# Kernel tuning notes

Measured on AMD Instinct MI355X. Metric: run time of the kernel, lower is better.

## Reference

```python
import jax, jax.numpy as jnp
import numpy as np

B, T, K, H = 32, 128, 16, 4   # batch, agents, in_dim, num_heads
A = 2                          # out_dim (action dim)
H1 = H2 = 256
LOG_STD_MIN, LOG_STD_MAX = -20.0, 2.0


def _linear_params(key, out_dim, in_dim, uniform_w=None):
    k1, k2 = jax.random.split(key)
    if uniform_w is not None:
        w = jax.random.uniform(k1, (out_dim, in_dim), minval=-uniform_w, maxval=uniform_w)
        b = jax.random.uniform(k2, (out_dim,), minval=-uniform_w, maxval=uniform_w)
    else:
        bound = 1.0 / np.sqrt(in_dim)
        w = jax.random.uniform(k1, (out_dim, in_dim), minval=-bound, maxval=bound)
        b = jax.random.uniform(k2, (out_dim,), minval=-bound, maxval=bound)
    return w.astype(jnp.float32), b.astype(jnp.float32)


def setup_inputs() -> dict:
    key = jax.random.key(0)
    ks = jax.random.split(key, 10)
    state = jax.random.normal(ks[0], (B, T, K), dtype=jnp.float32)
    eps = jax.random.normal(ks[1], (B, T, A), dtype=jnp.float32)
    Wq, bq = _linear_params(ks[2], K * H, K)
    Wk, bk = _linear_params(ks[3], K * H, K)
    Wv, bv = _linear_params(ks[4], K * H, K)
    W1, b1 = _linear_params(ks[5], H1, K * H + K)
    W2, b2 = _linear_params(ks[6], H2, H1)
    Wmu, bmu = _linear_params(ks[7], A, H2, uniform_w=0.003)
    Wls, bls = _linear_params(ks[8], A, H2, uniform_w=0.003)
    return {"state": state, "eps": eps, "Wq": Wq, "bq": bq, "Wk": Wk, "bk": bk,
            "Wv": Wv, "bv": bv, "W1": W1, "b1": b1, "W2": W2, "b2": b2,
            "Wmu": Wmu, "bmu": bmu, "Wls": Wls, "bls": bls}


def reference(state, eps, Wq, bq, Wk, bk, Wv, bv, W1, b1, W2, b2, Wmu, bmu, Wls, bls):
    b, t, k = state.shape
    h = H
    # rel[b,i,j] = state[b,j] - state[b,i]
    rel = state[:, None, :, :] - state[:, :, None, :]          # (b,t,t,k)
    q = jax.nn.relu(state @ Wq.T + bq).reshape(b, t, h, k)     # (b,t,h,k)
    q = q.transpose(0, 2, 1, 3)                                # (b,h,t,k)
    Kt = jax.nn.relu(rel @ Wk.T + bk).reshape(b, t, t, h, k)   # (b,i,j,h,k)
    V = jax.nn.relu(rel @ Wv.T + bv).reshape(b, t, t, h, k)
    # scores over pairwise keys vs per-agent query; softmax over j (dim=2 in torch)
    s = jnp.einsum('bijhk,bhik->bhij', Kt, q) / jnp.sqrt(jnp.float32(k))
    w = jax.nn.softmax(s, axis=3)                              # softmax over j
    x = jnp.einsum('bhij,bijhk->bhik', w, V)                   # (b,h,t,k)
    x = x.transpose(0, 2, 1, 3).reshape(b, t, h * k)           # (b,t,h*k)
    x = jnp.concatenate([x, state], axis=-1)                   # (b,t,h*k+k)
    x = jax.nn.relu(x @ W1.T + b1)
    x = jax.nn.relu(x @ W2.T + b2)
    mu = jnp.tanh(x @ Wmu.T + bmu)
    log_std = jnp.tanh(x @ Wls.T + bls)
    log_std = LOG_STD_MIN + 0.5 * (LOG_STD_MAX - LOG_STD_MIN) * (log_std + 1.0)
    std = jnp.exp(log_std)
    z = mu + std * eps                                         # rsample
    action = jnp.tanh(z)
    # Normal log_prob with (z-mu)/std == eps, minus tanh correction
    log_prob = (-0.5 * eps * eps - log_std - 0.5 * jnp.log(2.0 * jnp.pi)) \
               - jnp.log(1.0 - action * action + 1e-7)
    log_prob = jnp.sum(log_prob, axis=-1, keepdims=True)
    return action, log_prob
```

## Files before the change

### kernel.cpp

```cpp
#include <hip/hip_runtime.h>
#include <math.h>

#define NB 32
#define NT 128
#define KD 16

#define QG_OFF   0u
#define PKF_OFF  1048576u
#define PVT_OFF  3145728u
#define W1P_OFF  3670016u
#define W2P_OFF  3719168u

typedef float f32x4 __attribute__((ext_vector_type(4)));
typedef short bf16x8 __attribute__((ext_vector_type(8)));
typedef __fp16 f16x2 __attribute__((ext_vector_type(2)));
union U4B8 { uint4 u; bf16x8 h; };
union U4H8 { uint4 u; f16x2 h[4]; };

#define L_PK 0
#define L_PV 34816
#define L_P  52224
#define L_TOT 60928
#define L_X  0
#define L_H1 3584
#define L_H2 12032

__device__ __forceinline__ unsigned short bf16rne(float f) {
    unsigned u = __float_as_uint(f);
    return (unsigned short)((u + 0x7fffu + ((u >> 16) & 1u)) >> 16);
}
__device__ __forceinline__ void unpack8(uint4 u, float* f) {
    f[0] = __uint_as_float(u.x << 16); f[1] = __uint_as_float(u.x & 0xffff0000u);
    f[2] = __uint_as_float(u.y << 16); f[3] = __uint_as_float(u.y & 0xffff0000u);
    f[4] = __uint_as_float(u.z << 16); f[5] = __uint_as_float(u.z & 0xffff0000u);
    f[6] = __uint_as_float(u.w << 16); f[7] = __uint_as_float(u.w & 0xffff0000u);
}
__device__ __forceinline__ f16x2 pkmax(f16x2 a, f16x2 b) {
    f16x2 d;
    asm("v_pk_max_f16 %0, %1, %2" : "=v"(d) : "v"(a), "v"(b));
    return d;
}
#if __has_builtin(__builtin_amdgcn_fdot2)
#define FDOT2(a, b, c) __builtin_amdgcn_fdot2((a), (b), (c), false)
#else
#define FDOT2(a, b, c) ((c) + (float)(a)[0] * (float)(b)[0] + (float)(a)[1] * (float)(b)[1])
#endif

__global__ __launch_bounds__(256) void prep_kernel(
    const float* __restrict__ state,
    const float* __restrict__ Wq, const float* __restrict__ bq,
    const float* __restrict__ Wk, const float* __restrict__ Wv,
    const float* __restrict__ W1, const float* __restrict__ W2,
    char* __restrict__ wsb)
{
    const int blk = blockIdx.x, tid = threadIdx.x;
    float* Qg  = (float*)(wsb + QG_OFF);
    float* PkF = (float*)(wsb + PKF_OFF);
    unsigned short* PvT = (unsigned short*)(wsb + PVT_OFF);

    if (blk < 128) {
        __shared__ float Wl[3][64][17];
        __shared__ float Sl[32][17];
        const int b = blk >> 2, r0 = (blk & 3) * 32;
        for (int idx = tid; idx < 1024; idx += 256) {
            int o = idx >> 4, m = idx & 15;
            Wl[0][o][m] = Wq[idx];
            Wl[1][o][m] = Wk[idx];
            Wl[2][o][m] = Wv[idx];
        }
        for (int idx = tid; idx < 512; idx += 256)
            Sl[idx >> 4][idx & 15] = state[(size_t)(b * NT + r0) * KD + idx];
        __syncthreads();
        const int o = tid & 63, rr = tid >> 6;
        float wqv[16], wkv[16], wvv[16];
        #pragma unroll
        for (int m = 0; m < 16; ++m) {
            wqv[m] = Wl[0][o][m]; wkv[m] = Wl[1][o][m]; wvv[m] = Wl[2][o][m];
        }
        const float bqo = bq[o];
        for (int r = rr; r < 32; r += 4) {
            float aq = bqo, ak = 0.f, av = 0.f;
            #pragma unroll
            for (int m = 0; m < 16; ++m) {
                float s = Sl[r][m];
                aq = fmaf(s, wqv[m], aq);
                ak = fmaf(s, wkv[m], ak);
                av = fmaf(s, wvv[m], av);
            }
            int row = b * NT + r0 + r;
            Qg[row * 64 + o]  = fmaxf(aq, 0.f) * 0.25f;
            PkF[row * 64 + o] = ak;
            __fp16 hv = (__fp16)av;
            PvT[b * 8192 + o * NT + (r0 + r)] = *(unsigned short*)&hv;
        }
    } else if (blk < 140) {
        int fi = (blk - 128) * 256 + tid;
        int l = fi & 63, rest = fi >> 6;
        int t = rest & 15, ks = rest >> 4;
        int n = t * 16 + (l & 15);
        int kb = ks * 32 + (l >> 4) * 8;
        unsigned short v[8];
        #pragma unroll
        for (int j = 0; j < 8; ++j) {
            int k = kb + j;
            v[j] = (k < 80) ? bf16rne(W1[n * 80 + k]) : (unsigned short)0;
        }
        uint4 u;
        u.x = (unsigned)v[0] | ((unsigned)v[1] << 16);
        u.y = (unsigned)v[2] | ((unsigned)v[3] << 16);
        u.z = (unsigned)v[4] | ((unsigned)v[5] << 16);
        u.w = (unsigned)v[6] | ((unsigned)v[7] << 16);
        ((uint4*)(wsb + W1P_OFF))[fi] = u;
    } else {
        int fi = (blk - 140) * 256 + tid;
        int l = fi & 63, rest = fi >> 6;
        int t = rest & 15, ks = rest >> 4;
        int n = t * 16 + (l & 15);
        int kb = ks * 32 + (l >> 4) * 8;
        unsigned short v[8];
        #pragma unroll
        for (int j = 0; j < 8; ++j) v[j] = bf16rne(W2[n * 256 + kb + j]);
        uint4 u;
        u.x = (unsigned)v[0] | ((unsigned)v[1] << 16);
        u.y = (unsigned)v[2] | ((unsigned)v[3] << 16);
        u.z = (unsigned)v[4] | ((unsigned)v[5] << 16);
        u.w = (unsigned)v[6] | ((unsigned)v[7] << 16);
        ((uint4*)(wsb + W2P_OFF))[fi] = u;
    }
}

__global__ __launch_bounds__(512, 4) void actor_kernel(
    const float* __restrict__ state, const float* __restrict__ eps,
    const float* __restrict__ bkg, const float* __restrict__ bvg,
    const float* __restrict__ b1g, const float* __restrict__ b2g,
    const float* __restrict__ Wmu, const float* __restrict__ bmu,
    const float* __restrict__ Wls, const float* __restrict__ bls,
    const char* __restrict__ wsb, float* __restrict__ out)
{
    __shared__ __align__(16) char sm[L_TOT];
    float* smPk = (float*)(sm + L_PK);

    const int tid = threadIdx.x, w = tid >> 6, lane = tid & 63;
    const int bid = blockIdx.x;
    const int b    = (bid & 7) * 4 + ((bid >> 3) >> 4);
    const int tile = (bid >> 3) & 15;
    const int iloc = tile * 8 + w;
    const int row  = b * NT + iloc;
    const int h = lane >> 4, s = lane & 15, h16 = h << 4;
    const int g = h, lr = s;
    const int t0 = 2 * w;
    const int n0 = w * 32 + lr, n1 = n0 + 16;

    const float* Qg  = (const float*)(wsb + QG_OFF);
    const float* PkF = (const float*)(wsb + PKF_OFF);

    float qA[16], bkr[16];
    {
        const float4* qa  = (const float4*)(Qg + (size_t)row * 64 + h16);
        const float4* bk4 = (const float4*)(bkg + h16);
        #pragma unroll
        for (int q4 = 0; q4 < 4; ++q4) {
            float4 a = qa[q4], k4 = bk4[q4];
            qA[q4*4+0]=a.x; qA[q4*4+1]=a.y; qA[q4*4+2]=a.z; qA[q4*4+3]=a.w;
            bkr[q4*4+0]=k4.x; bkr[q4*4+1]=k4.y; bkr[q4*4+2]=k4.z; bkr[q4*4+3]=k4.w;
        }
    }
    const float bvo = bvg[lane];
    float stt = 0.f;
    if (tid < 128)
        stt = state[((size_t)b * NT + tile * 8 + (tid >> 4)) * KD + (tid & 15)];

    {
        const uint4* srcK = (const uint4*)(PkF + (size_t)b * NT * 64);
        #pragma unroll
        for (int it = 0; it < 4; ++it) {
            int idx = tid + it * 512;
            int r = idx >> 4, c = idx & 15;
            *(uint4*)(smPk + r * 68 + c * 4) = srcK[idx];
        }
        const uint4* srcV = (const uint4*)(wsb + PVT_OFF) + (size_t)b * 1024;
        #pragma unroll
        for (int it = 0; it < 2; ++it) {
            int idx = tid + it * 512;
            int o = idx >> 4, c = idx & 15;
            *(uint4*)(sm + L_PV + o * 272 + c * 16) = srcV[idx];
        }
    }
    __syncthreads();

    float mbeff[16], dotc = 0.f;
    {
        const float* pkI = smPk + iloc * 68 + h16;
        #pragma unroll
        for (int k = 0; k < 16; ++k) {
            float pk = pkI[k];
            mbeff[k] = pk - bkr[k];
            dotc = fmaf(qA[k], bkr[k] - pk, dotc);
        }
    }

    float sc[8];
    #pragma unroll
    for (int jj = 0; jj < 8; ++jj) {
        const float4* pk = (const float4*)(smPk + (s + (jj << 4)) * 68 + h16);
        float a = dotc;
        #pragma unroll
        for (int q4 = 0; q4 < 4; ++q4) {
            float4 v = pk[q4];
            float f[4] = {v.x, v.y, v.z, v.w};
            #pragma unroll
            for (int kk = 0; kk < 4; ++kk) {
                int k = q4 * 4 + kk;
                a = fmaf(qA[k], fmaxf(f[kk], mbeff[k]), a);
            }
        }
        sc[jj] = a;
    }

    float mx = sc[0];
    #pragma unroll
    for (int jj = 1; jj < 8; ++jj) mx = fmaxf(mx, sc[jj]);
    #pragma unroll
    for (int off = 1; off < 16; off <<= 1) mx = fmaxf(mx, __shfl_xor(mx, off));
    float l = 0.f;
    #pragma unroll
    for (int jj = 0; jj < 8; ++jj) { sc[jj] = __expf(sc[jj] - mx); l += sc[jj]; }
    #pragma unroll
    for (int off = 1; off < 16; off <<= 1) l += __shfl_xor(l, off);
    const float rl = 1.0f / l;
    {
        __fp16* prow = (__fp16*)(sm + L_P) + (w * 4 + h) * 136;
        #pragma unroll
        for (int jj = 0; jj < 8; ++jj) prow[(jj << 4) + s] = (__fp16)sc[jj];
    }
    asm volatile("s_waitcnt lgkmcnt(0)" ::: "memory");
    __builtin_amdgcn_sched_barrier(0);

    float xA;
    {
        const __fp16 pvi = *((const __fp16*)(sm + L_PV) + lane * 136 + iloc);
        const float mbvf = (float)pvi - bvo;
        const __fp16 mbvh = (__fp16)mbvf;
        const f16x2 mbv2 = {mbvh, mbvh};
        const uint4* vrow = (const uint4*)(sm + L_PV + lane * 272);
        const uint4* prow = (const uint4*)(sm + L_P + (w * 4 + h) * 272);
        float acc = 0.f;
        #pragma unroll
        for (int u = 0; u < 16; ++u) {
            U4H8 v; v.u = vrow[u];
            U4H8 p; p.u = prow[u];
            #pragma unroll
            for (int t = 0; t < 4; ++t)
                acc = FDOT2(p.h[t], pkmax(v.h[t], mbv2), acc);
        }
        xA = fmaf(rl, acc, -(float)mbvh);
    }
    __syncthreads();

    ((unsigned short*)(sm + L_X))[w * 104 + lane] = bf16rne(xA);
    if (tid < 128) {
        unsigned short* xr = (unsigned short*)(sm + L_X) + (tid >> 4) * 104;
        xr[64 + (tid & 15)] = bf16rne(stt);
        xr[80 + (tid & 15)] = 0;
    }
    if (tid < 384) {
        int r = 8 + tid / 48, c2 = (tid % 48) * 2;
        *(unsigned*)((unsigned short*)(sm + L_X) + r * 104 + c2) = 0u;
    }
    __syncthreads();

    const uint4* W1P = (const uint4*)(wsb + W1P_OFF);
    const uint4* W2P = (const uint4*)(wsb + W2P_OFF);

    {
        f32x4 a0 = {0.f, 0.f, 0.f, 0.f}, a1 = a0;
        #pragma unroll
        for (int ks = 0; ks < 3; ++ks) {
            U4B8 av; av.u = *(const uint4*)(sm + L_X + (lr * 104 + ks * 32 + g * 8) * 2);
            U4B8 b0; b0.u = W1P[((ks << 4) + t0) * 64 + lane];
            U4B8 b1; b1.u = W1P[((ks << 4) + t0 + 1) * 64 + lane];
            a0 = __builtin_amdgcn_mfma_f32_16x16x32_bf16(av.h, b0.h, a0, 0, 0, 0);
            a1 = __builtin_amdgcn_mfma_f32_16x16x32_bf16(av.h, b1.h, a1, 0, 0, 0);
        }
        const float bn0 = b1g[n0], bn1 = b1g[n1];
        #pragma unroll
        for (int qq = 0; qq < 4; ++qq) {
            *((unsigned short*)(sm + L_H1) + (4 * g + qq) * 264 + n0) =
                bf16rne(fmaxf(a0[qq] + bn0, 0.f));
            *((unsigned short*)(sm + L_H1) + (4 * g + qq) * 264 + n1) =
                bf16rne(fmaxf(a1[qq] + bn1, 0.f));
        }
    }
    __syncthreads();

    {
        f32x4 a0 = {0.f, 0.f, 0.f, 0.f}, a1 = a0;
        #pragma unroll
        for (int ks = 0; ks < 8; ++ks) {
            U4B8 av; av.u = *(const uint4*)(sm + L_H1 + (lr * 264 + ks * 32 + g * 8) * 2);
            U4B8 b0; b0.u = W2P[((ks << 4) + t0) * 64 + lane];
            U4B8 b1; b1.u = W2P[((ks << 4) + t0 + 1) * 64 + lane];
            a0 = __builtin_amdgcn_mfma_f32_16x16x32_bf16(av.h, b0.h, a0, 0, 0, 0);
            a1 = __builtin_amdgcn_mfma_f32_16x16x32_bf16(av.h, b1.h, a1, 0, 0, 0);
        }
        const float bn0 = b2g[n0], bn1 = b2g[n1];
        #pragma unroll
        for (int qq = 0; qq < 4; ++qq) {
            *((unsigned short*)(sm + L_H2) + (4 * g + qq) * 264 + n0) =
                bf16rne(fmaxf(a0[qq] + bn0, 0.f));
            *((unsigned short*)(sm + L_H2) + (4 * g + qq) * 264 + n1) =
                bf16rne(fmaxf(a1[qq] + bn1, 0.f));
        }
    }
    __syncthreads();

    {
        const int g2 = tid >> 4, m = g2 >> 2, d = g2 & 3, cc = tid & 15;
        const float* wrow = (d < 2) ? (Wmu + d * 256) : (Wls + (d - 2) * 256);
        float hbuf[16];
        uint4 ha = *(const uint4*)(sm + L_H2 + (m * 264 + cc * 16) * 2);
        uint4 hb = *(const uint4*)(sm + L_H2 + (m * 264 + cc * 16 + 8) * 2);
        unpack8(ha, hbuf); unpack8(hb, hbuf + 8);
        float dd = 0.f;
        #pragma unroll
        for (int kk = 0; kk < 16; ++kk)
            dd = fmaf(hbuf[kk], wrow[cc * 16 + kk], dd);
        #pragma unroll
        for (int off = 1; off < 16; off <<= 1) dd += __shfl_xor(dd, off);
        float* hd = (float*)(sm + L_P);
        if (cc == 0) {
            float bias = (d < 2) ? bmu[d] : bls[d - 2];
            hd[m * 4 + d] = tanhf(dd + bias);
        }
    }
    __syncthreads();
    if (tid < 8) {
        const float* hd = (const float*)(sm + L_P);
        const int m = tid;
        const int orow = b * NT + tile * 8 + m;
        float lp = 0.f;
        #pragma unroll
        for (int d = 0; d < 2; ++d) {
            float mu  = hd[m * 4 + d];
            float lsr = hd[m * 4 + 2 + d];
            float ls  = -20.f + 11.f * (lsr + 1.f);
            float e   = eps[orow * 2 + d];
            float z   = mu + __expf(ls) * e;
            float a   = tanhf(z);
            out[orow * 2 + d] = a;
            lp += -0.5f * e * e - ls - 0.91893853320467274f - __logf(1.f - a * a + 1e-7f);
        }
        out[NB * NT * 2 + orow] = lp;
    }
}

extern "C" void kernel_launch(void* const* d_in, const int* in_sizes, int n_in,
                              void* d_out, int out_size, void* d_ws, size_t ws_size,
                              hipStream_t stream) {
    const float* state = (const float*)d_in[0];
    const float* eps   = (const float*)d_in[1];
    const float* Wq    = (const float*)d_in[2];
    const float* bq    = (const float*)d_in[3];
    const float* Wk    = (const float*)d_in[4];
    const float* bk    = (const float*)d_in[5];
    const float* Wv    = (const float*)d_in[6];
    const float* bv    = (const float*)d_in[7];
    const float* W1    = (const float*)d_in[8];
    const float* b1    = (const float*)d_in[9];
    const float* W2    = (const float*)d_in[10];
    const float* b2    = (const float*)d_in[11];
    const float* Wmu   = (const float*)d_in[12];
    const float* bmu   = (const float*)d_in[13];
    const float* Wls   = (const float*)d_in[14];
    const float* bls   = (const float*)d_in[15];
    float* out = (float*)d_out;
    char* wsb  = (char*)d_ws;

    prep_kernel<<<172, 256, 0, stream>>>(state, Wq, bq, Wk, Wv, W1, W2, wsb);
    actor_kernel<<<512, 512, 0, stream>>>(state, eps, bk, bv, b1, b2,
                                          Wmu, bmu, Wls, bls, wsb, out);
}
```

Before: 22.77 us.

## Store keys in fp16, compute scores with packed dot2, prefetch MLP weights

The key projection is now written by the prep kernel as fp16 instead of fp32. This halves the global traffic and the LDS footprint for keys, and the attention scores are computed with packed f16 max and fdot2 instead of scalar fp32 FMAs. The LDS layout is reorganised so the X buffer gets its own region, which lets its zero-fill move to the prologue and removes one block barrier. W1 and half of W2 are prefetched into registers before they are needed, to hide global latency. The cost is reduced score precision in fp16 and higher register pressure.

```diff
diff --git a/kernel.cpp b/kernel.cpp
--- a/kernel.cpp
+++ b/kernel.cpp
@@ -6,10 +6,10 @@
 #define KD 16
 
 #define QG_OFF   0u
-#define PKF_OFF  1048576u
-#define PVT_OFF  3145728u
-#define W1P_OFF  3670016u
-#define W2P_OFF  3719168u
+#define PKH_OFF  1048576u
+#define PVT_OFF  1572864u
+#define W1P_OFF  2097152u
+#define W2P_OFF  2146304u
 
 typedef float f32x4 __attribute__((ext_vector_type(4)));
 typedef short bf16x8 __attribute__((ext_vector_type(8)));
@@ -18,12 +18,12 @@
 union U4H8 { uint4 u; f16x2 h[4]; };
 
 #define L_PK 0
-#define L_PV 34816
-#define L_P  52224
-#define L_TOT 60928
-#define L_X  0
-#define L_H1 3584
-#define L_H2 12032
+#define L_PV 18432
+#define L_P  35840
+#define L_X  44544
+#define L_TOT 47872
+#define L_H1 0
+#define L_H2 8448
 
 __device__ __forceinline__ unsigned short bf16rne(float f) {
     unsigned u = __float_as_uint(f);
@@ -54,8 +54,8 @@
     char* __restrict__ wsb)
 {
     const int blk = blockIdx.x, tid = threadIdx.x;
-    float* Qg  = (float*)(wsb + QG_OFF);
-    float* PkF = (float*)(wsb + PKF_OFF);
+    float* Qg = (float*)(wsb + QG_OFF);
+    unsigned short* PkH = (unsigned short*)(wsb + PKH_OFF);
     unsigned short* PvT = (unsigned short*)(wsb + PVT_OFF);
 
     if (blk < 128) {
@@ -88,10 +88,11 @@
                 av = fmaf(s, wvv[m], av);
             }
             int row = b * NT + r0 + r;
-            Qg[row * 64 + o]  = fmaxf(aq, 0.f) * 0.25f;
-            PkF[row * 64 + o] = ak;
+            Qg[row * 64 + o] = fmaxf(aq, 0.f) * 0.25f;
+            __fp16 hk = (__fp16)ak;
+            PkH[(size_t)b * 8192 + (r0 + r) * 64 + o] = *(unsigned short*)&hk;
             __fp16 hv = (__fp16)av;
-            PvT[b * 8192 + o * NT + (r0 + r)] = *(unsigned short*)&hv;
+            PvT[(size_t)b * 8192 + o * NT + (r0 + r)] = *(unsigned short*)&hv;
         }
     } else if (blk < 140) {
         int fi = (blk - 128) * 256 + tid;
@@ -138,7 +139,6 @@
     const char* __restrict__ wsb, float* __restrict__ out)
 {
     __shared__ __align__(16) char sm[L_TOT];
-    float* smPk = (float*)(sm + L_PK);
 
     const int tid = threadIdx.x, w = tid >> 6, lane = tid & 63;
     const int bid = blockIdx.x;
@@ -151,70 +151,84 @@
     const int t0 = 2 * w;
     const int n0 = w * 32 + lr, n1 = n0 + 16;
 
-    const float* Qg  = (const float*)(wsb + QG_OFF);
-    const float* PkF = (const float*)(wsb + PKF_OFF);
-
-    float qA[16], bkr[16];
+    const float* Qg = (const float*)(wsb + QG_OFF);
+
+    {
+        const uint4* srcK = (const uint4*)(wsb + PKH_OFF) + (size_t)b * 1024;
+        #pragma unroll
+        for (int it = 0; it < 2; ++it) {
+            int idx = tid + it * 512;
+            int r = idx >> 3, c = idx & 7;
+            *(uint4*)(sm + L_PK + r * 144 + c * 16) = srcK[idx];
+        }
+        const uint4* srcV = (const uint4*)(wsb + PVT_OFF) + (size_t)b * 1024;
+        #pragma unroll
+        for (int it = 0; it < 2; ++it) {
+            int idx = tid + it * 512;
+            int o = idx >> 4, c = idx & 15;
+            *(uint4*)(sm + L_PV + o * 272 + c * 16) = srcV[idx];
+        }
+        if (tid < 384) {
+            int r = 8 + tid / 48, c2 = (tid % 48) * 2;
+            *(unsigned*)((unsigned short*)(sm + L_X) + r * 104 + c2) = 0u;
+        }
+    }
+
+    float qf[16], bkf[16];
     {
         const float4* qa  = (const float4*)(Qg + (size_t)row * 64 + h16);
         const float4* bk4 = (const float4*)(bkg + h16);
         #pragma unroll
         for (int q4 = 0; q4 < 4; ++q4) {
             float4 a = qa[q4], k4 = bk4[q4];
-            qA[q4*4+0]=a.x; qA[q4*4+1]=a.y; qA[q4*4+2]=a.z; qA[q4*4+3]=a.w;
-            bkr[q4*4+0]=k4.x; bkr[q4*4+1]=k4.y; bkr[q4*4+2]=k4.z; bkr[q4*4+3]=k4.w;
+            qf[q4*4+0]=a.x; qf[q4*4+1]=a.y; qf[q4*4+2]=a.z; qf[q4*4+3]=a.w;
+            bkf[q4*4+0]=k4.x; bkf[q4*4+1]=k4.y; bkf[q4*4+2]=k4.z; bkf[q4*4+3]=k4.w;
         }
     }
     const float bvo = bvg[lane];
     float stt = 0.f;
     if (tid < 128)
         stt = state[((size_t)b * NT + tile * 8 + (tid >> 4)) * KD + (tid & 15)];
-
-    {
-        const uint4* srcK = (const uint4*)(PkF + (size_t)b * NT * 64);
-        #pragma unroll
-        for (int it = 0; it < 4; ++it) {
-            int idx = tid + it * 512;
-            int r = idx >> 4, c = idx & 15;
-            *(uint4*)(smPk + r * 68 + c * 4) = srcK[idx];
-        }
-        const uint4* srcV = (const uint4*)(wsb + PVT_OFF) + (size_t)b * 1024;
-        #pragma unroll
-        for (int it = 0; it < 2; ++it) {
-            int idx = tid + it * 512;
-            int o = idx >> 4, c = idx & 15;
-            *(uint4*)(sm + L_PV + o * 272 + c * 16) = srcV[idx];
-        }
-    }
     __syncthreads();
 
-    float mbeff[16], dotc = 0.f;
-    {
-        const float* pkI = smPk + iloc * 68 + h16;
-        #pragma unroll
-        for (int k = 0; k < 16; ++k) {
-            float pk = pkI[k];
-            mbeff[k] = pk - bkr[k];
-            dotc = fmaf(qA[k], bkr[k] - pk, dotc);
-        }
+    f16x2 q8[8], mb8[8];
+    float dotc;
+    {
+        U4H8 p0, p1;
+        p0.u = *(const uint4*)(sm + L_PK + iloc * 144 + h * 32);
+        p1.u = *(const uint4*)(sm + L_PK + iloc * 144 + h * 32 + 16);
+        #pragma unroll
+        for (int t = 0; t < 4; ++t) {
+            q8[t]     = __builtin_amdgcn_cvt_pkrtz(qf[2*t],   qf[2*t+1]);
+            q8[4 + t] = __builtin_amdgcn_cvt_pkrtz(qf[8+2*t], qf[8+2*t+1]);
+            f16x2 b0 = __builtin_amdgcn_cvt_pkrtz(bkf[2*t],   bkf[2*t+1]);
+            f16x2 b1 = __builtin_amdgcn_cvt_pkrtz(bkf[8+2*t], bkf[8+2*t+1]);
+            mb8[t]     = p0.h[t] - b0;
+            mb8[4 + t] = p1.h[t] - b1;
+        }
+        float d0 = 0.f, d1 = 0.f;
+        #pragma unroll
+        for (int t = 0; t < 4; ++t) {
+            d0 = FDOT2(q8[t],     mb8[t],     d0);
+            d1 = FDOT2(q8[4 + t], mb8[4 + t], d1);
+        }
+        dotc = -(d0 + d1);
     }
 
     float sc[8];
     #pragma unroll
     for (int jj = 0; jj < 8; ++jj) {
-        const float4* pk = (const float4*)(smPk + (s + (jj << 4)) * 68 + h16);
-        float a = dotc;
-        #pragma unroll
-        for (int q4 = 0; q4 < 4; ++q4) {
-            float4 v = pk[q4];
-            float f[4] = {v.x, v.y, v.z, v.w};
-            #pragma unroll
-            for (int kk = 0; kk < 4; ++kk) {
-                int k = q4 * 4 + kk;
-                a = fmaf(qA[k], fmaxf(f[kk], mbeff[k]), a);
-            }
-        }
-        sc[jj] = a;
+        const char* pr = sm + L_PK + (s + (jj << 4)) * 144 + h * 32;
+        U4H8 v0, v1;
+        v0.u = *(const uint4*)(pr);
+        v1.u = *(const uint4*)(pr + 16);
+        float aE = 0.f, aO = 0.f;
+        #pragma unroll
+        for (int t = 0; t < 4; ++t) {
+            aE = FDOT2(q8[t],     pkmax(v0.h[t], mb8[t]),     aE);
+            aO = FDOT2(q8[4 + t], pkmax(v1.h[t], mb8[4 + t]), aO);
+        }
+        sc[jj] = dotc + aE + aO;
     }
 
     float mx = sc[0];
@@ -235,6 +249,14 @@
     }
     asm volatile("s_waitcnt lgkmcnt(0)" ::: "memory");
     __builtin_amdgcn_sched_barrier(0);
+
+    const uint4* W1P = (const uint4*)(wsb + W1P_OFF);
+    uint4 w1f0[3], w1f1[3];
+    #pragma unroll
+    for (int ks = 0; ks < 3; ++ks) {
+        w1f0[ks] = W1P[((ks << 4) + t0) * 64 + lane];
+        w1f1[ks] = W1P[((ks << 4) + t0 + 1) * 64 + lane];
+    }
 
     float xA;
     {
@@ -255,7 +277,6 @@
         }
         xA = fmaf(rl, acc, -(float)mbvh);
     }
-    __syncthreads();
 
     ((unsigned short*)(sm + L_X))[w * 104 + lane] = bf16rne(xA);
     if (tid < 128) {
@@ -263,22 +284,22 @@
         xr[64 + (tid & 15)] = bf16rne(stt);
         xr[80 + (tid & 15)] = 0;
     }
-    if (tid < 384) {
-        int r = 8 + tid / 48, c2 = (tid % 48) * 2;
-        *(unsigned*)((unsigned short*)(sm + L_X) + r * 104 + c2) = 0u;
-    }
     __syncthreads();
 
-    const uint4* W1P = (const uint4*)(wsb + W1P_OFF);
     const uint4* W2P = (const uint4*)(wsb + W2P_OFF);
-
+    uint4 w2f0[4], w2f1[4];
+    #pragma unroll
+    for (int ks = 0; ks < 4; ++ks) {
+        w2f0[ks] = W2P[((ks << 4) + t0) * 64 + lane];
+        w2f1[ks] = W2P[((ks << 4) + t0 + 1) * 64 + lane];
+    }
     {
         f32x4 a0 = {0.f, 0.f, 0.f, 0.f}, a1 = a0;
         #pragma unroll
         for (int ks = 0; ks < 3; ++ks) {
             U4B8 av; av.u = *(const uint4*)(sm + L_X + (lr * 104 + ks * 32 + g * 8) * 2);
-            U4B8 b0; b0.u = W1P[((ks << 4) + t0) * 64 + lane];
-            U4B8 b1; b1.u = W1P[((ks << 4) + t0 + 1) * 64 + lane];
+            U4B8 b0; b0.u = w1f0[ks];
+            U4B8 b1; b1.u = w1f1[ks];
             a0 = __builtin_amdgcn_mfma_f32_16x16x32_bf16(av.h, b0.h, a0, 0, 0, 0);
             a1 = __builtin_amdgcn_mfma_f32_16x16x32_bf16(av.h, b1.h, a1, 0, 0, 0);
         }
@@ -296,7 +317,15 @@
     {
         f32x4 a0 = {0.f, 0.f, 0.f, 0.f}, a1 = a0;
         #pragma unroll
-        for (int ks = 0; ks < 8; ++ks) {
+        for (int ks = 0; ks < 4; ++ks) {
+            U4B8 av; av.u = *(const uint4*)(sm + L_H1 + (lr * 264 + ks * 32 + g * 8) * 2);
+            U4B8 b0; b0.u = w2f0[ks];
+            U4B8 b1; b1.u = w2f1[ks];
+            a0 = __builtin_amdgcn_mfma_f32_16x16x32_bf16(av.h, b0.h, a0, 0, 0, 0);
+            a1 = __builtin_amdgcn_mfma_f32_16x16x32_bf16(av.h, b1.h, a1, 0, 0, 0);
+        }
+        #pragma unroll
+        for (int ks = 4; ks < 8; ++ks) {
             U4B8 av; av.u = *(const uint4*)(sm + L_H1 + (lr * 264 + ks * 32 + g * 8) * 2);
             U4B8 b0; b0.u = W2P[((ks << 4) + t0) * 64 + lane];
             U4B8 b1; b1.u = W2P[((ks << 4) + t0 + 1) * 64 + lane];
```

Result: faster. 21.40 us (-6.0%).
